# Performance work log

Measured on AMD Instinct MI355X. Metric: run time of the kernel, lower is better.

The kernel has to match this reference:

```python
import jax, jax.numpy as jnp
import numpy as np

H = 5  # LSTM hidden size


def _lstm_layer(x, Wih, Whh, bih, bhh):
    # x: [B, T, D]; Wih: [4H, D]; Whh: [4H, H]; biases: [4H]
    B, T, _ = x.shape
    # precompute input contribution with one big GEMM (torch gate order i,f,g,o)
    xg = jnp.einsum('btd,gd->btg', x, Wih) + bih + bhh  # [B,T,4H]
    xg = jnp.swapaxes(xg, 0, 1)  # [T,B,4H]
    WhhT = Whh.T

    def step(carry, g_t):
        h, c = carry
        g = g_t + h @ WhhT
        i, f, gg, o = jnp.split(g, 4, axis=-1)
        i = jax.nn.sigmoid(i)
        f = jax.nn.sigmoid(f)
        gg = jnp.tanh(gg)
        o = jax.nn.sigmoid(o)
        c = f * c + i * gg
        h = o * jnp.tanh(c)
        return (h, c), h

    h0 = jnp.zeros((B, H), x.dtype)
    c0 = jnp.zeros((B, H), x.dtype)
    _, hs = jax.lax.scan(step, (h0, c0), xg)
    return jnp.swapaxes(hs, 0, 1)  # [B,T,H]


def _stacked_lstm(x, params):
    for (Wih, Whh, bih, bhh) in params:
        x = _lstm_layer(x, Wih, Whh, bih, bhh)
    return x


def setup_inputs() -> dict:
    key = jax.random.key(0)
    ks = jax.random.split(key, 24)
    B, T, D = 512, 1024, 225
    s = 1.0 / np.sqrt(H)

    def u(k, shape):
        return jax.random.uniform(k, shape, jnp.float32, -s, s)

    inp = {"x": jax.random.normal(ks[0], (B, T, D), jnp.float32)}
    # lstm1: layer0 input D=225, layer1 input H=5
    inp["l1_Wih0"] = u(ks[1], (4 * H, D)); inp["l1_Whh0"] = u(ks[2], (4 * H, H))
    inp["l1_bih0"] = u(ks[3], (4 * H,)); inp["l1_bhh0"] = u(ks[4], (4 * H,))
    inp["l1_Wih1"] = u(ks[5], (4 * H, H)); inp["l1_Whh1"] = u(ks[6], (4 * H, H))
    inp["l1_bih1"] = u(ks[7], (4 * H,)); inp["l1_bhh1"] = u(ks[8], (4 * H,))
    inp["fc1_W"] = u(ks[9], (H, H)); inp["fc1_b"] = u(ks[10], (H,))
    # lstm2: both layers input H=5
    inp["l2_Wih0"] = u(ks[11], (4 * H, H)); inp["l2_Whh0"] = u(ks[12], (4 * H, H))
    inp["l2_bih0"] = u(ks[13], (4 * H,)); inp["l2_bhh0"] = u(ks[14], (4 * H,))
    inp["l2_Wih1"] = u(ks[15], (4 * H, H)); inp["l2_Whh1"] = u(ks[16], (4 * H, H))
    inp["l2_bih1"] = u(ks[17], (4 * H,)); inp["l2_bhh1"] = u(ks[18], (4 * H,))
    inp["fc2_W"] = u(ks[19], (H, H)); inp["fc2_b"] = u(ks[20], (H,))
    return inp


def reference(x, l1_Wih0, l1_Whh0, l1_bih0, l1_bhh0,
              l1_Wih1, l1_Whh1, l1_bih1, l1_bhh1,
              fc1_W, fc1_b,
              l2_Wih0, l2_Whh0, l2_bih0, l2_bhh0,
              l2_Wih1, l2_Whh1, l2_bih1, l2_bhh1,
              fc2_W, fc2_b):
    # dropout layers are identity in inference mode
    h = _stacked_lstm(x, [(l1_Wih0, l1_Whh0, l1_bih0, l1_bhh0),
                          (l1_Wih1, l1_Whh1, l1_bih1, l1_bhh1)])
    h = jax.nn.relu(h @ fc1_W.T + fc1_b)
    h = _stacked_lstm(h, [(l2_Wih0, l2_Whh0, l2_bih0, l2_bhh0),
                          (l2_Wih1, l2_Whh1, l2_bih1, l2_bhh1)])
    return jax.nn.sigmoid(h @ fc2_W.T + fc2_b)
```

## Files before the change

### kernel.cpp

```cpp
#include <hip/hip_runtime.h>
#include <math.h>

#define T_STEPS 1024
#define B_SIZE  512
#define D_IN    225
#define WT_K    228
#define LOG2E   1.4426950408889634f

__device__ __forceinline__ float fexp2(float x) {
#if __has_builtin(__builtin_amdgcn_exp2f)
  return __builtin_amdgcn_exp2f(x);
#else
  return exp2f(x);
#endif
}
__device__ __forceinline__ float frcp(float x) {
#if __has_builtin(__builtin_amdgcn_rcpf)
  return __builtin_amdgcn_rcpf(x);
#else
  return 1.0f / x;
#endif
}
#define SIG(x) frcp(1.0f + fexp2((x) * (-LOG2E)))
#define TH(x)  fmaf(2.0f, frcp(1.0f + fexp2((x) * (-2.0f * LOG2E))), -1.0f)

#define GL16(gp, lp) __builtin_amdgcn_global_load_lds(                          \
    (const __attribute__((address_space(1))) void*)(gp),                        \
    (__attribute__((address_space(3))) void*)(lp), 16, 0, 0)
#define GL4(gp, lp)  __builtin_amdgcn_global_load_lds(                          \
    (const __attribute__((address_space(1))) void*)(gp),                        \
    (__attribute__((address_space(3))) void*)(lp), 4, 0, 0)

#define WAIT_VM0() do {                                                         \
    asm volatile("s_waitcnt vmcnt(0)" ::: "memory");                            \
    __builtin_amdgcn_sched_barrier(0);                                          \
  } while (0)
#define WAIT_VM10() do {                                                        \
    asm volatile("s_waitcnt vmcnt(10)" ::: "memory");                           \
    __builtin_amdgcn_sched_barrier(0);                                          \
  } while (0)

__global__ __launch_bounds__(256)
void prep_wt(const float* __restrict__ Wih, const float* __restrict__ bih,
             const float* __restrict__ bhh, float* __restrict__ wt2)
{
  int i = blockIdx.x * 256 + threadIdx.x;
  int g = i / WT_K, kk = i - g * WT_K;
  float v = 0.f;
  if (g < 20 && kk < 225) v = Wih[g * 225 + kk];
  if (i >= 4560 && i < 4580) v = bih[i - 4560] + bhh[i - 4560];
  wt2[i] = v;
}

__global__ __launch_bounds__(256)
void xg_gemm(const float* __restrict__ x, const float* __restrict__ wtg,
             float* __restrict__ xg)
{
  __shared__ __align__(16) float xs[64 * D_IN];
  __shared__ __align__(16) float wt[4608];
  const int tid  = threadIdx.x;
  const int lane = tid & 63;
  const int w    = __builtin_amdgcn_readfirstlane(tid >> 6);

  {
    int n0 = (w < 2) ? 5 : 4;
    int c0 = (w < 2) ? w * 5 : 10 + (w - 2) * 4;
    for (int m = 0; m < n0; ++m)
      GL16(wtg + (c0 + m) * 256 + lane * 4, wt + (c0 + m) * 256);
  }
  {
    const float* src = x + (size_t)blockIdx.x * (64 * D_IN);
    for (int m = 0; m < 14; ++m)
      GL16(src + (w * 14 + m) * 256 + lane * 4, xs + (w * 14 + m) * 256);
    if (w == 0) GL4(src + 14336 + lane, xs + 14336);
  }
  __syncthreads();

  const int row = lane;
  const float* xr = xs + row * D_IN;
  const float* wr = wt + (5 * w) * WT_K;
  float acc[5];
#pragma unroll
  for (int j = 0; j < 5; ++j) acc[j] = wt[4560 + 5 * w + j];

#pragma unroll 8
  for (int kb = 0; kb < 224; kb += 4) {
    float x0 = xr[kb], x1 = xr[kb + 1], x2 = xr[kb + 2], x3 = xr[kb + 3];
#pragma unroll
    for (int j = 0; j < 5; ++j) {
      const float4 wv = *(const float4*)(wr + j * WT_K + kb);
      acc[j] = fmaf(x0, wv.x, acc[j]);
      acc[j] = fmaf(x1, wv.y, acc[j]);
      acc[j] = fmaf(x2, wv.z, acc[j]);
      acc[j] = fmaf(x3, wv.w, acc[j]);
    }
  }
  {
    float xl = xr[224];
#pragma unroll
    for (int j = 0; j < 5; ++j) acc[j] = fmaf(xl, wr[j * WT_K + 224], acc[j]);
  }
  float* op = xg + ((size_t)blockIdx.x * 64 + row) * 20 + w;
#pragma unroll
  for (int j = 0; j < 5; ++j) op[4 * j] = acc[j];
}

__global__ __launch_bounds__(64)
void lstm_fused(const float* __restrict__ xg, float* __restrict__ out,
              const float* __restrict__ l1_Whh0,
              const float* __restrict__ l1_Wih1, const float* __restrict__ l1_Whh1,
              const float* __restrict__ l1_bih1, const float* __restrict__ l1_bhh1,
              const float* __restrict__ fc1_W,  const float* __restrict__ fc1_b,
              const float* __restrict__ l2_Wih0, const float* __restrict__ l2_Whh0,
              const float* __restrict__ l2_bih0, const float* __restrict__ l2_bhh0,
              const float* __restrict__ l2_Wih1, const float* __restrict__ l2_Whh1,
              const float* __restrict__ l2_bih1, const float* __restrict__ l2_bhh1,
              const float* __restrict__ fc2_W,  const float* __restrict__ fc2_b)
{
  __shared__ __align__(16) float xq[2][2][1280];
  __shared__ float outb[2][64][5];
  __shared__ __align__(16) float hx[128];
  const int lane  = threadIdx.x & 63;
  const int half  = lane >> 5;
  const int l32   = lane & 31;
  const int stage = (l32 < 30) ? (l32 / 5) : 6;
  const int u     = (l32 < 30) ? (l32 - stage * 5) : 0;
  const int b0    = blockIdx.x * 2;

  const bool is_l0   = (stage == 0);
  const bool is_relu = (stage == 2);
  const bool is_fc   = (stage == 2) || (stage == 5);
  const bool is_fc2  = (stage == 5);

  float wi[4][5] = {}, wh[4][5] = {}, bs[4] = {};
  if (stage == 0) {
#pragma unroll
    for (int q = 0; q < 4; ++q)
#pragma unroll
      for (int j = 0; j < 5; ++j) wh[q][j] = l1_Whh0[(u + 5 * q) * 5 + j];
  } else if (stage == 1) {
#pragma unroll
    for (int q = 0; q < 4; ++q) {
#pragma unroll
      for (int j = 0; j < 5; ++j) {
        wi[q][j] = l1_Wih1[(u + 5 * q) * 5 + j];
        wh[q][j] = l1_Whh1[(u + 5 * q) * 5 + j];
      }
      bs[q] = l1_bih1[u + 5 * q] + l1_bhh1[u + 5 * q];
    }
  } else if (stage == 3) {
#pragma unroll
    for (int q = 0; q < 4; ++q) {
#pragma unroll
      for (int j = 0; j < 5; ++j) {
        wi[q][j] = l2_Wih0[(u + 5 * q) * 5 + j];
        wh[q][j] = l2_Whh0[(u + 5 * q) * 5 + j];
      }
      bs[q] = l2_bih0[u + 5 * q] + l2_bhh0[u + 5 * q];
    }
  } else if (stage == 4) {
#pragma unroll
    for (int q = 0; q < 4; ++q) {
#pragma unroll
      for (int j = 0; j < 5; ++j) {
        wi[q][j] = l2_Wih1[(u + 5 * q) * 5 + j];
        wh[q][j] = l2_Whh1[(u + 5 * q) * 5 + j];
      }
      bs[q] = l2_bih1[u + 5 * q] + l2_bhh1[u + 5 * q];
    }
  } else if (stage == 2) {
#pragma unroll
    for (int j = 0; j < 5; ++j) wi[0][j] = fc1_W[u * 5 + j];
    bs[0] = fc1_b[u];
  } else if (stage == 5) {
#pragma unroll
    for (int j = 0; j < 5; ++j) wi[0][j] = fc2_W[u * 5 + j];
    bs[0] = fc2_b[u];
  }

  float* hxp = hx;
  const int woff = half * 64 + stage * 8 + u;
  const int ioff = half * 64 + ((stage > 0) ? stage - 1 : 0) * 8;
  const int hoff = half * 64 + stage * 8;

  for (int i = lane; i < 128; i += 64) hxp[i] = 0.f;

  const float* src0 = xg + (size_t)(b0 + 0) * T_STEPS * 20;
  const float* src1 = xg + (size_t)(b0 + 1) * T_STEPS * 20;

#define STAGE_CHUNK(CH, BUF)                                                   \
  { const float* s0_ = src0 + (CH) * 1280;                                     \
    const float* s1_ = src1 + (CH) * 1280;                                     \
    float* d0_ = &xq[BUF][0][0];                                               \
    float* d1_ = &xq[BUF][1][0];                                               \
    _Pragma("unroll")                                                          \
    for (int m = 0; m < 5; ++m) {                                              \
      GL16(s0_ + m * 256 + lane * 4, d0_ + m * 256);                           \
      GL16(s1_ + m * 256 + lane * 4, d1_ + m * 256);                           \
    } }

#define TICKX(KK, XQB, GUARDED, KVAL)                                          \
  { hxp[woff] = hv;                               \
    const float4 iv  = *(const float4*)(hxp + ioff);                           \
    const float  in4 = hxp[ioff + 4];                                          \
    const float4 hv4 = *(const float4*)(hxp + hoff);                           \
    const float  hh4 = hxp[hoff + 4];                                          \
    const float4 Qv  = *(const float4*)((XQB) + 20 * (KK));                    \
    const float inx[5] = {iv.x, iv.y, iv.z, iv.w, in4};                        \
    const float hhx[5] = {hv4.x, hv4.y, hv4.z, hv4.w, hh4};                    \
    float pre[4];                                                              \
    pre[0] = is_l0 ? Qv.x : bs[0];                                             \
    pre[1] = is_l0 ? Qv.y : bs[1];                                             \
    pre[2] = is_l0 ? Qv.z : bs[2];                                             \
    pre[3] = is_l0 ? Qv.w : bs[3];                                             \
    _Pragma("unroll")                                                          \
    for (int q = 0; q < 4; ++q) {                                              \
      _Pragma("unroll")                                                        \
      for (int j = 0; j < 5; ++j) pre[q] = fmaf(wi[q][j], inx[j], pre[q]);     \
      _Pragma("unroll")                                                        \
      for (int j = 0; j < 5; ++j) pre[q] = fmaf(wh[q][j], hhx[j], pre[q]);     \
    }                                                                          \
    float i_ = SIG(pre[0]), f_ = SIG(pre[1]);                                  \
    float g_ = TH(pre[2]),  o_ = SIG(pre[3]);                                  \
    float cn = fmaf(f_, c, i_ * g_);                                           \
    float hl = o_ * TH(cn);                                                    \
    float fx = is_relu ? fmaxf(pre[0], 0.0f) : i_;                             \
    float hn = is_fc ? fx : hl;                                                \
    if (GUARDED) { bool ok = (KVAL) >= stage; c = ok ? cn : c; hv = ok ? hn : hv; } \
    else         { c = cn; hv = hn; }                                          \
    if (is_fc2) outb[half][((KK) + 59) & 63][u] = i_;                          \
  }

#define FLUSH(TBASE)                                                           \
  { _Pragma("unroll")                                                          \
    for (int i2 = 0; i2 < 10; ++i2) {                                          \
      int idx = i2 * 64 + lane;                                                \
      int e  = (idx >= 320) ? 1 : 0;                                           \
      int r  = idx - e * 320;                                                  \
      int tq = r / 5;                                                          \
      int j2 = r - tq * 5;                                                     \
      int tt = (TBASE) + tq;                                                   \
      float v = outb[e][tt & 63][j2];                                          \
      if (tt >= 0 && tt < T_STEPS)                                             \
        out[((size_t)(b0 + e) * T_STEPS + tt) * 5 + j2] = v;                   \
    } }

  float hv = 0.f, c = 0.f;

  STAGE_CHUNK(0, 0)
  WAIT_VM0();

  {
    STAGE_CHUNK(1, 1)
    const float* xqb = &xq[0][half][4 * u];
    for (int kk = 0; kk < 5; ++kk) TICKX(kk, xqb, true, kk)
#pragma unroll 4
    for (int kk = 5; kk < 64; ++kk) TICKX(kk, xqb, false, 0)
    FLUSH(-5)
    WAIT_VM10();
  }
  for (int ch = 1; ch < 16; ++ch) {
    if (ch < 15) STAGE_CHUNK(ch + 1, (ch + 1) & 1)
    const float* xqb = &xq[ch & 1][half][4 * u];
#pragma unroll 4
    for (int kk = 0; kk < 64; ++kk) TICKX(kk, xqb, false, 0)
    FLUSH(ch * 64 - 5)
    WAIT_VM10();
  }
  {
    const float* xqb = &xq[0][half][4 * u];
    for (int kk = 0; kk < 5; ++kk) TICKX(kk, xqb, false, 0)
    FLUSH(T_STEPS - 5)
  }

#undef STAGE_CHUNK
#undef TICKX
#undef FLUSH
}

extern "C" void kernel_launch(void* const* d_in, const int* in_sizes, int n_in,
                              void* d_out, int out_size, void* d_ws, size_t ws_size,
                              hipStream_t stream)
{
  const float* x        = (const float*)d_in[0];
  const float* l1_Wih0  = (const float*)d_in[1];
  const float* l1_Whh0  = (const float*)d_in[2];
  const float* l1_bih0  = (const float*)d_in[3];
  const float* l1_bhh0  = (const float*)d_in[4];
  const float* l1_Wih1  = (const float*)d_in[5];
  const float* l1_Whh1  = (const float*)d_in[6];
  const float* l1_bih1  = (const float*)d_in[7];
  const float* l1_bhh1  = (const float*)d_in[8];
  const float* fc1_W    = (const float*)d_in[9];
  const float* fc1_b    = (const float*)d_in[10];
  const float* l2_Wih0  = (const float*)d_in[11];
  const float* l2_Whh0  = (const float*)d_in[12];
  const float* l2_bih0  = (const float*)d_in[13];
  const float* l2_bhh0  = (const float*)d_in[14];
  const float* l2_Wih1  = (const float*)d_in[15];
  const float* l2_Whh1  = (const float*)d_in[16];
  const float* l2_bih1  = (const float*)d_in[17];
  const float* l2_bhh1  = (const float*)d_in[18];
  const float* fc2_W    = (const float*)d_in[19];
  const float* fc2_b    = (const float*)d_in[20];

  float* xg   = (float*)d_ws;
  float* wtws = xg + 10485760;
  float* out  = (float*)d_out;

  prep_wt<<<dim3(18), dim3(256), 0, stream>>>(l1_Wih0, l1_bih0, l1_bhh0, wtws);

  xg_gemm<<<dim3((B_SIZE * T_STEPS) / 64), dim3(256), 0, stream>>>(x, wtws, xg);

  lstm_fused<<<dim3(B_SIZE / 2), dim3(64), 0, stream>>>(
      xg, out, l1_Whh0, l1_Wih1, l1_Whh1, l1_bih1, l1_bhh1,
      fc1_W, fc1_b, l2_Wih0, l2_Whh0, l2_bih0, l2_bhh0,
      l2_Wih1, l2_Whh1, l2_bih1, l2_bhh1, fc2_W, fc2_b);
}
```

Before: 422.7 us.

## Exchange LSTM hidden states via ds_bpermute and read GEMM weights from global

The fused LSTM kernel's per-step hidden-state exchange no longer goes through a shared-memory scratch array. Each lane now gathers its five input and five recurrent values directly from other lanes with ds_bpermute, which is meant to remove the write/read round trip on the serial recurrence path. Separately, the input-projection GEMM stops staging the weight matrix in LDS and reads it straight from global/cache, with a smaller unroll. That trades LDS footprint and staging loads for scalar or cached global weight reads in the inner loop.

```diff
diff --git a/kernel.cpp b/kernel.cpp
--- a/kernel.cpp
+++ b/kernel.cpp
@@ -57,33 +57,26 @@
              float* __restrict__ xg)
 {
   __shared__ __align__(16) float xs[64 * D_IN];
-  __shared__ __align__(16) float wt[4608];
   const int tid  = threadIdx.x;
   const int lane = tid & 63;
-  const int w    = __builtin_amdgcn_readfirstlane(tid >> 6);
-
-  {
-    int n0 = (w < 2) ? 5 : 4;
-    int c0 = (w < 2) ? w * 5 : 10 + (w - 2) * 4;
-    for (int m = 0; m < n0; ++m)
-      GL16(wtg + (c0 + m) * 256 + lane * 4, wt + (c0 + m) * 256);
-  }
+  const int w    = tid >> 6;
+
   {
     const float* src = x + (size_t)blockIdx.x * (64 * D_IN);
+#pragma unroll
     for (int m = 0; m < 14; ++m)
       GL16(src + (w * 14 + m) * 256 + lane * 4, xs + (w * 14 + m) * 256);
     if (w == 0) GL4(src + 14336 + lane, xs + 14336);
   }
   __syncthreads();
 
-  const int row = lane;
-  const float* xr = xs + row * D_IN;
-  const float* wr = wt + (5 * w) * WT_K;
+  const float* wr = wtg + (5 * w) * WT_K;
   float acc[5];
 #pragma unroll
-  for (int j = 0; j < 5; ++j) acc[j] = wt[4560 + 5 * w + j];
-
-#pragma unroll 8
+  for (int j = 0; j < 5; ++j) acc[j] = wtg[4560 + 5 * w + j];
+  const float* xr = xs + lane * D_IN;
+
+#pragma unroll 4
   for (int kb = 0; kb < 224; kb += 4) {
     float x0 = xr[kb], x1 = xr[kb + 1], x2 = xr[kb + 2], x3 = xr[kb + 3];
 #pragma unroll
@@ -100,7 +93,7 @@
 #pragma unroll
     for (int j = 0; j < 5; ++j) acc[j] = fmaf(xl, wr[j * WT_K + 224], acc[j]);
   }
-  float* op = xg + ((size_t)blockIdx.x * 64 + row) * 20 + w;
+  float* op = xg + ((size_t)blockIdx.x * 64 + lane) * 20 + w;
 #pragma unroll
   for (int j = 0; j < 5; ++j) op[4 * j] = acc[j];
 }
@@ -119,7 +112,6 @@
 {
   __shared__ __align__(16) float xq[2][2][1280];
   __shared__ float outb[2][64][5];
-  __shared__ __align__(16) float hx[128];
   const int lane  = threadIdx.x & 63;
   const int half  = lane >> 5;
   const int l32   = lane & 31;
@@ -178,12 +170,15 @@
     bs[0] = fc2_b[u];
   }
 
-  float* hxp = hx;
-  const int woff = half * 64 + stage * 8 + u;
-  const int ioff = half * 64 + ((stage > 0) ? stage - 1 : 0) * 8;
-  const int hoff = half * 64 + stage * 8;
-
-  for (int i = lane; i < 128; i += 64) hxp[i] = 0.f;
+  int ii[5], ih[5];
+  const int bse = half * 32;
+  const int inb = (stage >= 1 && stage <= 5) ? (stage - 1) * 5 : 0;
+  const int hb_ = (stage <= 5) ? stage * 5 : 0;
+#pragma unroll
+  for (int j = 0; j < 5; ++j) {
+    ii[j] = (bse + inb + j) * 4;
+    ih[j] = (bse + hb_ + j) * 4;
+  }
 
   const float* src0 = xg + (size_t)(b0 + 0) * T_STEPS * 20;
   const float* src1 = xg + (size_t)(b0 + 1) * T_STEPS * 20;
@@ -199,15 +194,15 @@
       GL16(s1_ + m * 256 + lane * 4, d1_ + m * 256);                           \
     } }
 
-#define TICKX(KK, XQB, GUARDED, KVAL)                                          \
-  { hxp[woff] = hv;                               \
-    const float4 iv  = *(const float4*)(hxp + ioff);                           \
-    const float  in4 = hxp[ioff + 4];                                          \
-    const float4 hv4 = *(const float4*)(hxp + hoff);                           \
-    const float  hh4 = hxp[hoff + 4];                                          \
-    const float4 Qv  = *(const float4*)((XQB) + 20 * (KK));                    \
-    const float inx[5] = {iv.x, iv.y, iv.z, iv.w, in4};                        \
-    const float hhx[5] = {hv4.x, hv4.y, hv4.z, hv4.w, hh4};                    \
+#define TICKB(KK, XQB, GUARDED, KVAL)                                          \
+  { const int hvi_ = __float_as_int(hv);                                       \
+    float inx[5], hhx[5];                                                      \
+    _Pragma("unroll")                                                          \
+    for (int j = 0; j < 5; ++j) {                                              \
+      inx[j] = __int_as_float(__builtin_amdgcn_ds_bpermute(ii[j], hvi_));      \
+      hhx[j] = __int_as_float(__builtin_amdgcn_ds_bpermute(ih[j], hvi_));      \
+    }                                                                          \
+    const float4 Qv = *(const float4*)((XQB) + 20 * (KK));                     \
     float pre[4];                                                              \
     pre[0] = is_l0 ? Qv.x : bs[0];                                             \
     pre[1] = is_l0 ? Qv.y : bs[1];                                             \
@@ -253,9 +248,9 @@
   {
     STAGE_CHUNK(1, 1)
     const float* xqb = &xq[0][half][4 * u];
-    for (int kk = 0; kk < 5; ++kk) TICKX(kk, xqb, true, kk)
+    for (int kk = 0; kk < 5; ++kk) TICKB(kk, xqb, true, kk)
 #pragma unroll 4
-    for (int kk = 5; kk < 64; ++kk) TICKX(kk, xqb, false, 0)
+    for (int kk = 5; kk < 64; ++kk) TICKB(kk, xqb, false, 0)
     FLUSH(-5)
     WAIT_VM10();
   }
@@ -263,18 +258,18 @@
     if (ch < 15) STAGE_CHUNK(ch + 1, (ch + 1) & 1)
     const float* xqb = &xq[ch & 1][half][4 * u];
 #pragma unroll 4
-    for (int kk = 0; kk < 64; ++kk) TICKX(kk, xqb, false, 0)
+    for (int kk = 0; kk < 64; ++kk) TICKB(kk, xqb, false, 0)
     FLUSH(ch * 64 - 5)
     WAIT_VM10();
   }
   {
     const float* xqb = &xq[0][half][4 * u];
-    for (int kk = 0; kk < 5; ++kk) TICKX(kk, xqb, false, 0)
+    for (int kk = 0; kk < 5; ++kk) TICKB(kk, xqb, false, 0)
     FLUSH(T_STEPS - 5)
   }
 
 #undef STAGE_CHUNK
-#undef TICKX
+#undef TICKB
 #undef FLUSH
 }
 
```

New measurement: 602.4 us. 1.43x slower.
